# Optimization experiments

Measured on AMD Instinct MI355X. Metric: run time of the kernel, lower is better.

The kernel has to match this reference:

```python
import jax, jax.numpy as jnp
import numpy as np

N = 50000      # nodes
E = 800000     # edges (before self-loops)
IN = 128       # in_dim
OUT = 128      # out_dim
H = 4          # heads
C = OUT // H   # per-head channels
G = 64         # number of graphs in batch
NEG_SLOPE = 0.2
GN_EPS = 1e-5


def setup_inputs() -> dict:
    key = jax.random.key(0)
    ks = jax.random.split(key, 6)
    x = jax.random.normal(ks[0], (N, IN), dtype=jnp.float32)
    edge_index = jax.random.randint(ks[1], (2, E), 0, N, dtype=jnp.int32)
    batch = jnp.sort(jax.random.randint(ks[2], (N,), 0, G, dtype=jnp.int32))
    # glorot-ish init for GATv2 params
    s = float(np.sqrt(6.0 / (IN + H * C)))
    Wl = jax.random.uniform(ks[3], (IN, H * C), jnp.float32, -s, s)  # source (lin_l)
    Wr = jax.random.uniform(ks[4], (IN, H * C), jnp.float32, -s, s)  # target (lin_r)
    sa = float(np.sqrt(6.0 / (C + 1)))
    att = jax.random.uniform(ks[5], (H, C), jnp.float32, -sa, sa)
    bias_conv = jnp.zeros((H * C,), jnp.float32)
    gn_weight = jnp.ones((OUT,), jnp.float32)
    gn_bias = jnp.zeros((OUT,), jnp.float32)
    gn_mean_scale = jnp.ones((OUT,), jnp.float32)
    return {"x": x, "edge_index": edge_index, "batch": batch,
            "Wl": Wl, "Wr": Wr, "att": att, "bias_conv": bias_conv,
            "gn_weight": gn_weight, "gn_bias": gn_bias, "gn_mean_scale": gn_mean_scale}


def reference(x, edge_index, batch, Wl, Wr, att, bias_conv, gn_weight, gn_bias, gn_mean_scale):
    n = x.shape[0]
    # --- GATv2Conv (eval: dropout off), add_self_loops=True ---
    loop = jnp.arange(n, dtype=edge_index.dtype)
    src = jnp.concatenate([edge_index[0], loop])  # source j
    dst = jnp.concatenate([edge_index[1], loop])  # target i
    xl = (x @ Wl).reshape(n, H, C)  # source-side features
    xr = (x @ Wr).reshape(n, H, C)  # target-side features
    m = xl[src] + xr[dst]                               # [E', H, C]
    e = jax.nn.leaky_relu(m, NEG_SLOPE)
    logits = jnp.einsum('ehc,hc->eh', e, att)           # [E', H]
    # segment softmax over destination nodes
    amax = jax.ops.segment_max(logits, dst, num_segments=n)   # [N, H]
    ex = jnp.exp(logits - amax[dst])
    denom = jax.ops.segment_sum(ex, dst, num_segments=n)      # [N, H]
    alpha = ex / (denom[dst] + 1e-16)
    out = jax.ops.segment_sum(alpha[:, :, None] * xl[src], dst, num_segments=n)  # [N, H, C]
    out = out.reshape(n, H * C) + bias_conv
    # --- GraphNorm: (x - a*mean_g) / sqrt(var_g + eps) * w + b ---
    ones = jnp.ones((n, 1), out.dtype)
    cnt = jnp.maximum(jax.ops.segment_sum(ones, batch, num_segments=G), 1.0)  # [G, 1]
    mean = jax.ops.segment_sum(out, batch, num_segments=G) / cnt             # [G, OUT]
    out_c = out - mean[batch] * gn_mean_scale
    var = jax.ops.segment_sum(out_c * out_c, batch, num_segments=G) / cnt    # [G, OUT]
    y = out_c / jnp.sqrt(var[batch] + GN_EPS) * gn_weight + gn_bias
    # --- ELU ---
    return jax.nn.elu(y)
```

## Files before the change

### kernel.cpp

```cpp
#include <hip/hip_runtime.h>
#include <math.h>

#define HH 4
#define GG 64
#define CHUNK 64
#define BDST 16
#define BSH  4
#define SLOT 768
#define NPT  16
#define HWORDS 3328
constexpr float NEG_SLOPE = 0.2f;
constexpr float GN_EPS = 1e-5f;

typedef __attribute__((ext_vector_type(8))) short bf16x8;
typedef __attribute__((ext_vector_type(4))) float f32x4;

__device__ __forceinline__ unsigned short f2bf_rne(float f) {
  unsigned u = __float_as_uint(f);
  u += 0x7fffu + ((u >> 16) & 1u);
  return (unsigned short)(u >> 16);
}

__global__ __launch_bounds__(256) void wpack(
    const float* __restrict__ Wl, const float* __restrict__ Wr,
    unsigned short* __restrict__ Bfrag) {
  int tid = blockIdx.x * 256 + threadIdx.x;
  int f = tid >> 6, l = tid & 63;
  int m = f >> 5;
  int t = (f >> 2) & 7;
  int ks = f & 3;
  int col = t * 16 + (l & 15);
  int k0 = ks * 32 + (l >> 4) * 8;
  const float* W = m ? Wr : Wl;
  unsigned short* dst = Bfrag + ((size_t)f * 64 + l) * 8;
  #pragma unroll
  for (int j = 0; j < 8; ++j)
    dst[j] = f2bf_rne(W[(k0 + j) * 128 + col]);
}

__global__ __launch_bounds__(256) void prep_merged(
    const int* __restrict__ ei, int* __restrict__ gcur, int* __restrict__ ebuf,
    int E, int E2, int nbk, int SB,
    const float* __restrict__ x, const unsigned short* __restrict__ Bfrag,
    unsigned short* __restrict__ xlb, float* __restrict__ xr, int n) {
  __shared__ int hist[HWORDS];
  const int t = threadIdx.x;
  if ((int)blockIdx.x < SB) {
    for (int i = t; i < HWORDS; i += 256) hist[i] = 0;
    __syncthreads();
    unsigned wcache[NPT];
    const int base = blockIdx.x * (256 * NPT);
    #pragma unroll
    for (int i = 0; i < NPT; ++i) {
      int e = base + i * 256 + t;
      unsigned w = 0xFFFFFFFFu;
      if (e < E2) {
        int src, dst;
        if (e < E) { src = ei[e]; dst = ei[E + e]; }
        else       { src = e - E; dst = e - E; }
        w = ((unsigned)(dst >> BSH) << 20) | ((unsigned)(dst & (BDST - 1)) << 16)
            | (unsigned)src;
        atomicAdd(&hist[dst >> BSH], 1);
      }
      wcache[i] = w;
    }
    __syncthreads();
    for (int b = t; b < nbk; b += 256) {
      int c = hist[b];
      if (c) hist[b] = atomicAdd(&gcur[b], c);
    }
    __syncthreads();
    #pragma unroll
    for (int i = 0; i < NPT; ++i) {
      unsigned w = wcache[i];
      if (w == 0xFFFFFFFFu) continue;
      int b = w >> 20;
      int pos = atomicAdd(&hist[b], 1);
      if (pos < SLOT) ebuf[b * SLOT + pos] = (int)(w & 0xFFFFF);
    }
    return;
  }
  const int wave = ((blockIdx.x - SB) * 256 + t) >> 6;
  if (wave * 16 >= n) return;
  const int l = t & 63;
  const int arow = min(wave * 16 + (l & 15), n - 1);
  const float4* xrow = reinterpret_cast<const float4*>(x + (size_t)arow * 128);

  bf16x8 a[4];
  #pragma unroll
  for (int ks = 0; ks < 4; ++ks) {
    float4 lo = xrow[ks * 8 + (l >> 4) * 2];
    float4 hi = xrow[ks * 8 + (l >> 4) * 2 + 1];
    bf16x8 v;
    v[0] = (short)f2bf_rne(lo.x); v[1] = (short)f2bf_rne(lo.y);
    v[2] = (short)f2bf_rne(lo.z); v[3] = (short)f2bf_rne(lo.w);
    v[4] = (short)f2bf_rne(hi.x); v[5] = (short)f2bf_rne(hi.y);
    v[6] = (short)f2bf_rne(hi.z); v[7] = (short)f2bf_rne(hi.w);
    a[ks] = v;
  }

  const int r0 = wave * 16 + (l >> 4) * 4;
  const int cb = l & 15;
  #pragma unroll
  for (int tt = 0; tt < 8; ++tt) {
    f32x4 acc = {0.f, 0.f, 0.f, 0.f};
    #pragma unroll
    for (int ks = 0; ks < 4; ++ks) {
      const bf16x8* bp = reinterpret_cast<const bf16x8*>(
          Bfrag + ((size_t)((0 * 8 + tt) * 4 + ks) * 64 + l) * 8);
      acc = __builtin_amdgcn_mfma_f32_16x16x32_bf16(a[ks], *bp, acc, 0, 0, 0);
    }
    #pragma unroll
    for (int j = 0; j < 4; ++j) {
      int r = r0 + j;
      if (r < n) xlb[(size_t)r * 128 + tt * 16 + cb] = f2bf_rne(acc[j]);
    }
  }
  #pragma unroll
  for (int tt = 0; tt < 8; ++tt) {
    f32x4 acc = {0.f, 0.f, 0.f, 0.f};
    #pragma unroll
    for (int ks = 0; ks < 4; ++ks) {
      const bf16x8* bp = reinterpret_cast<const bf16x8*>(
          Bfrag + ((size_t)((1 * 8 + tt) * 4 + ks) * 64 + l) * 8);
      acc = __builtin_amdgcn_mfma_f32_16x16x32_bf16(a[ks], *bp, acc, 0, 0, 0);
    }
    #pragma unroll
    for (int j = 0; j < 4; ++j) {
      int r = r0 + j;
      if (r < n) xr[(size_t)r * 128 + tt * 16 + cb] = acc[j];
    }
  }
}

__global__ __launch_bounds__(256) void fused_aggr(
    const int* __restrict__ gcur, const int* __restrict__ ebuf,
    const unsigned char* __restrict__ xb,
    const float* __restrict__ xr, const float* __restrict__ att,
    float* __restrict__ out, int n) {
  __shared__ int eraw[SLOT];
  __shared__ int elist[SLOT + 16];
  __shared__ int ldeg[BDST];
  __shared__ int lrow[BDST + 1];
  __shared__ int lcur[BDST];
  const int b = blockIdx.x;
  const int t = threadIdx.x;
  const int cnt = min(gcur[b], SLOT);
  if (t < BDST) ldeg[t] = 0;
  __syncthreads();
  for (int i = t; i < cnt; i += 256) {
    int w = ebuf[b * SLOT + i];
    eraw[i] = w;
    atomicAdd(&ldeg[(w >> 16) & (BDST - 1)], 1);
  }
  __syncthreads();
  if (t < BDST) {
    int v = ldeg[t];
    int incl = v;
    #pragma unroll
    for (int d = 1; d < BDST; d <<= 1) {
      int u = __shfl_up(incl, d);
      if (t >= d) incl += u;
    }
    lrow[t] = incl - v;
    lcur[t] = incl - v;
    if (t == BDST - 1) lrow[BDST] = incl;
  }
  __syncthreads();
  for (int i = t; i < cnt; i += 256) {
    int w = eraw[i];
    int pos = atomicAdd(&lcur[(w >> 16) & (BDST - 1)], 1);
    elist[pos] = (w & 0xFFFF) << 8;
  }
  if (t < 16) elist[cnt + t] = 0;
  __syncthreads();

  const int wv = t >> 6, lane = t & 63;
  const int u = lane & 15, gi = lane >> 4;
  const float4 atA = *reinterpret_cast<const float4*>(att + u * 8);
  const float4 atB = *reinterpret_cast<const float4*>(att + u * 8 + 4);

  #define LDE(st) (*reinterpret_cast<const uint4*>( \
      xb + (size_t)(unsigned)ep[4 * (st) + gi] + u * 16))
  #define STEP(V, ebase) { \
    float x0 = __uint_as_float((V).x << 16); \
    float x1 = __uint_as_float((V).x & 0xffff0000u); \
    float x2 = __uint_as_float((V).y << 16); \
    float x3 = __uint_as_float((V).y & 0xffff0000u); \
    float x4 = __uint_as_float((V).z << 16); \
    float x5 = __uint_as_float((V).z & 0xffff0000u); \
    float x6 = __uint_as_float((V).w << 16); \
    float x7 = __uint_as_float((V).w & 0xffff0000u); \
    float t0 = x0 + xrA.x; t0 = fmaxf(t0, NEG_SLOPE * t0); \
    float t1 = x1 + xrA.y; t1 = fmaxf(t1, NEG_SLOPE * t1); \
    float t2 = x2 + xrA.z; t2 = fmaxf(t2, NEG_SLOPE * t2); \
    float t3 = x3 + xrA.w; t3 = fmaxf(t3, NEG_SLOPE * t3); \
    float t4 = x4 + xrB.x; t4 = fmaxf(t4, NEG_SLOPE * t4); \
    float t5 = x5 + xrB.y; t5 = fmaxf(t5, NEG_SLOPE * t5); \
    float t6 = x6 + xrB.z; t6 = fmaxf(t6, NEG_SLOPE * t6); \
    float t7 = x7 + xrB.w; t7 = fmaxf(t7, NEG_SLOPE * t7); \
    float p = t0 * atA.x; \
    p = fmaf(t1, atA.y, p); p = fmaf(t2, atA.z, p); p = fmaf(t3, atA.w, p); \
    p = fmaf(t4, atB.x, p); p = fmaf(t5, atB.y, p); p = fmaf(t6, atB.z, p); \
    p = fmaf(t7, atB.w, p); \
    p += __shfl_xor(p, 1); \
    p += __shfl_xor(p, 2); \
    float w = ((ebase) + gi < deg) ? __expf(p) : 0.f; \
    s += w; \
    a0 = fmaf(w, x0, a0); a1 = fmaf(w, x1, a1); \
    a2 = fmaf(w, x2, a2); a3 = fmaf(w, x3, a3); \
    a4 = fmaf(w, x4, a4); a5 = fmaf(w, x5, a5); \
    a6 = fmaf(w, x6, a6); a7 = fmaf(w, x7, a7); }

  for (int j = 0; j < 4; ++j) {
    const int ldst = wv * 4 + j;
    const int node = b * BDST + ldst;
    if (node >= n) break;
    const float4 xrA = *reinterpret_cast<const float4*>(xr + (size_t)node * 128 + u * 8);
    const float4 xrB = *reinterpret_cast<const float4*>(xr + (size_t)node * 128 + u * 8 + 4);
    const int k0 = lrow[ldst];
    const int deg = lrow[ldst + 1] - k0;
    const int* ep = elist + k0;

    uint4 V0 = LDE(0), V1 = LDE(1), V2 = LDE(2);
    float s = 0.f;
    float a0 = 0.f, a1 = 0.f, a2 = 0.f, a3 = 0.f;
    float a4 = 0.f, a5 = 0.f, a6 = 0.f, a7 = 0.f;
    const int S = (deg + 3) >> 2;
    for (int i = 0; i < S; ++i) {
      uint4 C = V0; V0 = V1; V1 = V2;
      if (4 * i + 12 < deg) V2 = LDE(i + 3);
      STEP(C, 4 * i)
    }
    s  += __shfl_xor(s, 16);  s  += __shfl_xor(s, 32);
    a0 += __shfl_xor(a0, 16); a0 += __shfl_xor(a0, 32);
    a1 += __shfl_xor(a1, 16); a1 += __shfl_xor(a1, 32);
    a2 += __shfl_xor(a2, 16); a2 += __shfl_xor(a2, 32);
    a3 += __shfl_xor(a3, 16); a3 += __shfl_xor(a3, 32);
    a4 += __shfl_xor(a4, 16); a4 += __shfl_xor(a4, 32);
    a5 += __shfl_xor(a5, 16); a5 += __shfl_xor(a5, 32);
    a6 += __shfl_xor(a6, 16); a6 += __shfl_xor(a6, 32);
    a7 += __shfl_xor(a7, 16); a7 += __shfl_xor(a7, 32);
    float inv = 1.f / (s + 1e-16f);
    if (gi == 0) {
      float* op = out + (size_t)node * 128 + u * 8;
      *reinterpret_cast<float4*>(op) =
          make_float4(a0 * inv, a1 * inv, a2 * inv, a3 * inv);
      *reinterpret_cast<float4*>(op + 4) =
          make_float4(a4 * inv, a5 * inv, a6 * inv, a7 * inv);
    }
  }
  #undef STEP
  #undef LDE
}

__global__ __launch_bounds__(128) void gn_stats(
    const float* __restrict__ out, const float* __restrict__ bias,
    const int* __restrict__ batch, float* __restrict__ gsum,
    float* __restrict__ gsumsq, int* __restrict__ gcnt, int n) {
  const int c = threadIdx.x;
  const int n0 = blockIdx.x * CHUNK;
  const int n1 = min(n0 + CHUNK, n);
  const float bc = bias[c];
  float bsum = 0.f, bsq = 0.f;
  int cnt = 0;
  int curg = batch[n0];
  for (int nid = n0; nid < n1; ++nid) {
    int g = batch[nid];
    if (g != curg) {
      atomicAdd(&gsum[curg * 128 + c], bsum);
      atomicAdd(&gsumsq[curg * 128 + c], bsq);
      if (c == 0) atomicAdd(&gcnt[curg], cnt);
      bsum = 0.f; bsq = 0.f; cnt = 0; curg = g;
    }
    float v = out[(size_t)nid * 128 + c] + bc;
    bsum += v; bsq += v * v; ++cnt;
  }
  atomicAdd(&gsum[curg * 128 + c], bsum);
  atomicAdd(&gsumsq[curg * 128 + c], bsq);
  if (c == 0) atomicAdd(&gcnt[curg], cnt);
}

__global__ __launch_bounds__(128) void gn_prep(
    const float* __restrict__ gsum, const float* __restrict__ gsumsq,
    const int* __restrict__ gcnt, const float* __restrict__ bias,
    const float* __restrict__ msc, const float* __restrict__ w,
    const float* __restrict__ b, float* __restrict__ K, float* __restrict__ S) {
  int g = blockIdx.x, c = threadIdx.x;
  float cnt = (float)max(gcnt[g], 1);
  float mean = gsum[g * 128 + c] / cnt;
  float a = msc[c];
  float var = gsumsq[g * 128 + c] / cnt - mean * mean * (2.f * a - a * a);
  float k = rsqrtf(var + GN_EPS) * w[c];
  K[g * 128 + c] = k;
  S[g * 128 + c] = (bias[c] - mean * a) * k + b[c];
}

__global__ __launch_bounds__(256) void gn_norm(
    float* __restrict__ out, const int* __restrict__ batch,
    const float* __restrict__ K, const float* __restrict__ S, int n) {
  int i = blockIdx.x * 256 + threadIdx.x;
  if (i >= n * 32) return;
  int nid = i >> 5, c4 = (i & 31) * 4;
  int g = batch[nid];
  const float4 k4 = *reinterpret_cast<const float4*>(K + g * 128 + c4);
  const float4 s4 = *reinterpret_cast<const float4*>(S + g * 128 + c4);
  float* op = out + (size_t)nid * 128 + c4;
  float4 v = *reinterpret_cast<const float4*>(op);
  v.x = fmaf(v.x, k4.x, s4.x); v.x = (v.x > 0.f) ? v.x : (__expf(v.x) - 1.f);
  v.y = fmaf(v.y, k4.y, s4.y); v.y = (v.y > 0.f) ? v.y : (__expf(v.y) - 1.f);
  v.z = fmaf(v.z, k4.z, s4.z); v.z = (v.z > 0.f) ? v.z : (__expf(v.z) - 1.f);
  v.w = fmaf(v.w, k4.w, s4.w); v.w = (v.w > 0.f) ? v.w : (__expf(v.w) - 1.f);
  *reinterpret_cast<float4*>(op) = v;
}

extern "C" void kernel_launch(void* const* d_in, const int* in_sizes, int n_in,
                              void* d_out, int out_size, void* d_ws, size_t ws_size,
                              hipStream_t stream) {
  const float* x    = (const float*)d_in[0];
  const int*   ei   = (const int*)d_in[1];
  const int*   batch= (const int*)d_in[2];
  const float* Wl   = (const float*)d_in[3];
  const float* Wr   = (const float*)d_in[4];
  const float* att  = (const float*)d_in[5];
  const float* bias = (const float*)d_in[6];
  const float* gw   = (const float*)d_in[7];
  const float* gb   = (const float*)d_in[8];
  const float* gms  = (const float*)d_in[9];
  float* out = (float*)d_out;

  const int n  = in_sizes[0] / 128;
  const int E  = in_sizes[1] / 2;
  const int E2 = E + n;
  const int NBK = (n + BDST - 1) / BDST;
  const int SB = (E2 + 256 * NPT - 1) / (256 * NPT);
  const int GB = (((n + 15) / 16) * 64 + 255) / 256;

  char* ws = (char*)d_ws;
  size_t off = 0;
  int*   gcur    = (int*)(ws + off); off += (size_t)((NBK + 63) & ~63) * 4;
  int*   gcnt    = (int*)(ws + off); off += GG * 4;
  float* gsum    = (float*)(ws + off); off += GG * 128 * 4;
  float* gsumsq  = (float*)(ws + off); off += GG * 128 * 4;
  size_t zero_bytes = off;
  int*   ebuf    = (int*)(ws + off); off += (size_t)NBK * SLOT * 4;
  unsigned short* xlb = (unsigned short*)(ws + off); off += (size_t)n * 128 * 2;
  float* xr      = (float*)(ws + off); off += (size_t)n * 128 * 4;
  unsigned short* Bfrag = (unsigned short*)(ws + off); off += 64 * 64 * 8 * 2;
  float* gK      = (float*)(ws + off); off += GG * 128 * 4;
  float* gS      = (float*)(ws + off); off += GG * 128 * 4;

  hipMemsetAsync(ws, 0, zero_bytes, stream);

  wpack<<<16, 256, 0, stream>>>(Wl, Wr, (unsigned short*)Bfrag);

  prep_merged<<<SB + GB, 256, 0, stream>>>(ei, gcur, ebuf, E, E2, NBK, SB,
                                           x, Bfrag, xlb, xr, n);

  fused_aggr<<<NBK, 256, 0, stream>>>(gcur, ebuf, (const unsigned char*)xlb,
                                      xr, att, out, n);

  gn_stats<<<(n + CHUNK - 1) / CHUNK, 128, 0, stream>>>(out, bias, batch, gsum, gsumsq, gcnt, n);
  gn_prep<<<GG, 128, 0, stream>>>(gsum, gsumsq, gcnt, bias, gms, gw, gb, gK, gS);

  gn_norm<<<(n * 32 + 255) / 256, 256, 0, stream>>>(out, batch, gK, gS, n);
}
```

Measured before the change: 116.9 us.

## Split leaky-ReLU logits into per-node linear terms plus an abs term

```diff
diff --git a/kernel.cpp b/kernel.cpp
--- a/kernel.cpp
+++ b/kernel.cpp
@@ -42,7 +42,9 @@
     const int* __restrict__ ei, int* __restrict__ gcur, int* __restrict__ ebuf,
     int E, int E2, int nbk, int SB,
     const float* __restrict__ x, const unsigned short* __restrict__ Bfrag,
-    unsigned short* __restrict__ xlb, float* __restrict__ xr, int n) {
+    const float* __restrict__ att,
+    unsigned short* __restrict__ xlb, unsigned short* __restrict__ xrb,
+    float* __restrict__ dA, float* __restrict__ dB, int n) {
   __shared__ int hist[HWORDS];
   const int t = threadIdx.x;
   if ((int)blockIdx.x < SB) {
@@ -101,6 +103,7 @@
 
   const int r0 = wave * 16 + (l >> 4) * 4;
   const int cb = l & 15;
+  float pd[4] = {0.f, 0.f, 0.f, 0.f};
   #pragma unroll
   for (int tt = 0; tt < 8; ++tt) {
     f32x4 acc = {0.f, 0.f, 0.f, 0.f};
@@ -110,10 +113,23 @@
           Bfrag + ((size_t)((0 * 8 + tt) * 4 + ks) * 64 + l) * 8);
       acc = __builtin_amdgcn_mfma_f32_16x16x32_bf16(a[ks], *bp, acc, 0, 0, 0);
     }
+    float attv = att[tt * 16 + cb];
     #pragma unroll
     for (int j = 0; j < 4; ++j) {
       int r = r0 + j;
-      if (r < n) xlb[(size_t)r * 128 + tt * 16 + cb] = f2bf_rne(acc[j]);
+      unsigned short h = f2bf_rne(acc[j]);
+      if (r < n) xlb[(size_t)r * 128 + tt * 16 + cb] = h;
+      pd[j] = fmaf(__uint_as_float((unsigned)h << 16), attv, pd[j]);
+    }
+    if (tt & 1) {
+      #pragma unroll
+      for (int j = 0; j < 4; ++j) {
+        float v = pd[j];
+        #pragma unroll
+        for (int mk = 1; mk < 16; mk <<= 1) v += __shfl_xor(v, mk);
+        if (cb == 0 && r0 + j < n) dA[(size_t)(r0 + j) * 4 + (tt >> 1)] = v;
+        pd[j] = 0.f;
+      }
     }
   }
   #pragma unroll
@@ -125,10 +141,23 @@
           Bfrag + ((size_t)((1 * 8 + tt) * 4 + ks) * 64 + l) * 8);
       acc = __builtin_amdgcn_mfma_f32_16x16x32_bf16(a[ks], *bp, acc, 0, 0, 0);
     }
+    float attv = att[tt * 16 + cb];
     #pragma unroll
     for (int j = 0; j < 4; ++j) {
       int r = r0 + j;
-      if (r < n) xr[(size_t)r * 128 + tt * 16 + cb] = acc[j];
+      unsigned short h = f2bf_rne(acc[j]);
+      if (r < n) xrb[(size_t)r * 128 + tt * 16 + cb] = h;
+      pd[j] = fmaf(__uint_as_float((unsigned)h << 16), attv, pd[j]);
+    }
+    if (tt & 1) {
+      #pragma unroll
+      for (int j = 0; j < 4; ++j) {
+        float v = pd[j];
+        #pragma unroll
+        for (int mk = 1; mk < 16; mk <<= 1) v += __shfl_xor(v, mk);
+        if (cb == 0 && r0 + j < n) dB[(size_t)(r0 + j) * 4 + (tt >> 1)] = v;
+        pd[j] = 0.f;
+      }
     }
   }
 }
@@ -136,8 +165,9 @@
 __global__ __launch_bounds__(256) void fused_aggr(
     const int* __restrict__ gcur, const int* __restrict__ ebuf,
     const unsigned char* __restrict__ xb,
-    const float* __restrict__ xr, const float* __restrict__ att,
-    float* __restrict__ out, int n) {
+    const unsigned char* __restrict__ xrb,
+    const float* __restrict__ dA, const float* __restrict__ dB,
+    const float* __restrict__ att, float* __restrict__ out, int n) {
   __shared__ int eraw[SLOT];
   __shared__ int elist[SLOT + 16];
   __shared__ int ldeg[BDST];
@@ -177,12 +207,14 @@
 
   const int wv = t >> 6, lane = t & 63;
   const int u = lane & 15, gi = lane >> 4;
+  const int hh = u >> 2;
   const float4 atA = *reinterpret_cast<const float4*>(att + u * 8);
   const float4 atB = *reinterpret_cast<const float4*>(att + u * 8 + 4);
 
   #define LDE(st) (*reinterpret_cast<const uint4*>( \
       xb + (size_t)(unsigned)ep[4 * (st) + gi] + u * 16))
-  #define STEP(V, ebase) { \
+  #define LDA(st) (dA[((unsigned)ep[4 * (st) + gi] >> 8) * 4 + hh])
+  #define STEP(V, da, ebase) { \
     float x0 = __uint_as_float((V).x << 16); \
     float x1 = __uint_as_float((V).x & 0xffff0000u); \
     float x2 = __uint_as_float((V).y << 16); \
@@ -191,21 +223,18 @@
     float x5 = __uint_as_float((V).z & 0xffff0000u); \
     float x6 = __uint_as_float((V).w << 16); \
     float x7 = __uint_as_float((V).w & 0xffff0000u); \
-    float t0 = x0 + xrA.x; t0 = fmaxf(t0, NEG_SLOPE * t0); \
-    float t1 = x1 + xrA.y; t1 = fmaxf(t1, NEG_SLOPE * t1); \
-    float t2 = x2 + xrA.z; t2 = fmaxf(t2, NEG_SLOPE * t2); \
-    float t3 = x3 + xrA.w; t3 = fmaxf(t3, NEG_SLOPE * t3); \
-    float t4 = x4 + xrB.x; t4 = fmaxf(t4, NEG_SLOPE * t4); \
-    float t5 = x5 + xrB.y; t5 = fmaxf(t5, NEG_SLOPE * t5); \
-    float t6 = x6 + xrB.z; t6 = fmaxf(t6, NEG_SLOPE * t6); \
-    float t7 = x7 + xrB.w; t7 = fmaxf(t7, NEG_SLOPE * t7); \
-    float p = t0 * atA.x; \
-    p = fmaf(t1, atA.y, p); p = fmaf(t2, atA.z, p); p = fmaf(t3, atA.w, p); \
-    p = fmaf(t4, atB.x, p); p = fmaf(t5, atB.y, p); p = fmaf(t6, atB.z, p); \
-    p = fmaf(t7, atB.w, p); \
+    float p = fabsf(x0 + xr0) * atA.x; \
+    p = fmaf(fabsf(x1 + xr1), atA.y, p); \
+    p = fmaf(fabsf(x2 + xr2), atA.z, p); \
+    p = fmaf(fabsf(x3 + xr3), atA.w, p); \
+    p = fmaf(fabsf(x4 + xr4), atB.x, p); \
+    p = fmaf(fabsf(x5 + xr5), atB.y, p); \
+    p = fmaf(fabsf(x6 + xr6), atB.z, p); \
+    p = fmaf(fabsf(x7 + xr7), atB.w, p); \
     p += __shfl_xor(p, 1); \
     p += __shfl_xor(p, 2); \
-    float w = ((ebase) + gi < deg) ? __expf(p) : 0.f; \
+    float lg = fmaf(0.4f, p, fmaf(0.6f, (da), eB)); \
+    float w = ((ebase) + gi < deg) ? __expf(lg) : 0.f; \
     s += w; \
     a0 = fmaf(w, x0, a0); a1 = fmaf(w, x1, a1); \
     a2 = fmaf(w, x2, a2); a3 = fmaf(w, x3, a3); \
@@ -216,21 +245,31 @@
     const int ldst = wv * 4 + j;
     const int node = b * BDST + ldst;
     if (node >= n) break;
-    const float4 xrA = *reinterpret_cast<const float4*>(xr + (size_t)node * 128 + u * 8);
-    const float4 xrB = *reinterpret_cast<const float4*>(xr + (size_t)node * 128 + u * 8 + 4);
+    const uint4 xv = *reinterpret_cast<const uint4*>(xrb + (size_t)node * 256 + u * 16);
+    const float xr0 = __uint_as_float(xv.x << 16);
+    const float xr1 = __uint_as_float(xv.x & 0xffff0000u);
+    const float xr2 = __uint_as_float(xv.y << 16);
+    const float xr3 = __uint_as_float(xv.y & 0xffff0000u);
+    const float xr4 = __uint_as_float(xv.z << 16);
+    const float xr5 = __uint_as_float(xv.z & 0xffff0000u);
+    const float xr6 = __uint_as_float(xv.w << 16);
+    const float xr7 = __uint_as_float(xv.w & 0xffff0000u);
+    const float eB = 0.6f * dB[(size_t)node * 4 + hh];
     const int k0 = lrow[ldst];
     const int deg = lrow[ldst + 1] - k0;
     const int* ep = elist + k0;
 
     uint4 V0 = LDE(0), V1 = LDE(1), V2 = LDE(2);
+    float d0 = LDA(0), d1 = LDA(1), d2 = LDA(2);
     float s = 0.f;
     float a0 = 0.f, a1 = 0.f, a2 = 0.f, a3 = 0.f;
     float a4 = 0.f, a5 = 0.f, a6 = 0.f, a7 = 0.f;
     const int S = (deg + 3) >> 2;
     for (int i = 0; i < S; ++i) {
-      uint4 C = V0; V0 = V1; V1 = V2;
-      if (4 * i + 12 < deg) V2 = LDE(i + 3);
-      STEP(C, 4 * i)
+      uint4 C = V0; float dc = d0;
+      V0 = V1; V1 = V2; d0 = d1; d1 = d2;
+      V2 = LDE(i + 3); d2 = LDA(i + 3);
+      STEP(C, dc, 4 * i)
     }
     s  += __shfl_xor(s, 16);  s  += __shfl_xor(s, 32);
     a0 += __shfl_xor(a0, 16); a0 += __shfl_xor(a0, 32);
@@ -251,6 +290,7 @@
     }
   }
   #undef STEP
+  #undef LDA
   #undef LDE
 }
 
@@ -345,7 +385,9 @@
   size_t zero_bytes = off;
   int*   ebuf    = (int*)(ws + off); off += (size_t)NBK * SLOT * 4;
   unsigned short* xlb = (unsigned short*)(ws + off); off += (size_t)n * 128 * 2;
-  float* xr      = (float*)(ws + off); off += (size_t)n * 128 * 4;
+  unsigned short* xrb = (unsigned short*)(ws + off); off += (size_t)n * 128 * 2;
+  float* dA      = (float*)(ws + off); off += (size_t)((n + 63) & ~63) * 4 * 4;
+  float* dB      = (float*)(ws + off); off += (size_t)((n + 63) & ~63) * 4 * 4;
   unsigned short* Bfrag = (unsigned short*)(ws + off); off += 64 * 64 * 8 * 2;
   float* gK      = (float*)(ws + off); off += GG * 128 * 4;
   float* gS      = (float*)(ws + off); off += GG * 128 * 4;
@@ -355,10 +397,11 @@
   wpack<<<16, 256, 0, stream>>>(Wl, Wr, (unsigned short*)Bfrag);
 
   prep_merged<<<SB + GB, 256, 0, stream>>>(ei, gcur, ebuf, E, E2, NBK, SB,
-                                           x, Bfrag, xlb, xr, n);
+                                           x, Bfrag, att, xlb, xrb, dA, dB, n);
 
   fused_aggr<<<NBK, 256, 0, stream>>>(gcur, ebuf, (const unsigned char*)xlb,
-                                      xr, att, out, n);
+                                      (const unsigned char*)xrb, dA, dB,
+                                      att, out, n);
 
   gn_stats<<<(n + CHUNK - 1) / CHUNK, 128, 0, stream>>>(out, bias, batch, gsum, gsumsq, gcnt, n);
   gn_prep<<<GG, 128, 0, stream>>>(gsum, gsumsq, gcnt, bias, gms, gw, gb, gK, gS);
```

After: 116.1 us. About the same (-0.7%).
